# Kernel optimization log

Hardware: AMD Instinct MI355X
Metric: run time of the kernel (lower is better)

The kernel has to match this reference:

```python
import jax, jax.numpy as jnp
import numpy as np
from jax import lax

B, H = 4, 256          # batch, imsize
M1, M2 = 4096, 512     # total clusters at pooling level 1 / 2
E1, E2 = 65536, 8192   # coarsened edge counts
F = 64                 # node_feat_size (hard-coded in source)
HID = 100              # FCBlock hidden_ch


def _segment_mean(x, seg, n):
    s = jax.ops.segment_sum(x, seg, num_segments=n)
    c = jax.ops.segment_sum(jnp.ones((x.shape[0], 1), x.dtype), seg, num_segments=n)
    return s / jnp.maximum(c, 1.0)


def _fcblock(x, wi, bi, wh, bh, wo, bo):
    # FCBlock(hidden_ch=100, num_hidden_layers=3, outermost_linear=True)
    x = jax.nn.relu(x @ wi + bi)
    for k in range(wh.shape[0]):
        x = jax.nn.relu(x @ wh[k] + bh[k])
    return x @ wo + bo


def _graph_conv(x, ei, w_nei, w_self, b):
    # PyG GraphConv with aggr='mean': W_nei * mean_j x_j + W_self * x + b
    m = _segment_mean(x[ei[0]], ei[1], x.shape[0])
    return m @ w_nei + x @ w_self + b


def _render_qtr(G, feats):
    # feats: [N,20] = [centers(2), 3 channels x 6 quadratic params]
    centers = feats[:, :2]
    paras = feats[:, 2:].reshape(-1, 3, 6)
    dx = (G[:, 0] - centers[:, 0])[:, None]  # [N,1]
    dy = (G[:, 1] - centers[:, 1])[:, None]
    a, ah, aw, ahh, aww, ahw = (paras[:, :, k] for k in range(6))  # each [N,3]
    return a + ah * dx + aw * dy + ahh * dx ** 2 + aww * dy ** 2 + ahw * dx * dy


def setup_inputs() -> dict:
    key = jax.random.key(0)
    ks = iter(jax.random.split(key, 40))
    s = jnp.float32(0.05)
    d = {}
    d['img'] = jax.random.normal(next(ks), (B, H, H, 3), jnp.float32)
    d['conv_w'] = jax.random.normal(next(ks), (3, 3, 3, F), jnp.float32) * s
    d['conv_b'] = jax.random.normal(next(ks), (F,), jnp.float32) * s
    for p, din, dout in (('t1', F + 4, F), ('t2', F + 4, F), ('q', F, 18)):
        d[p + '_wi'] = jax.random.normal(next(ks), (din, HID), jnp.float32) * s
        d[p + '_bi'] = jax.random.normal(next(ks), (HID,), jnp.float32) * s
        d[p + '_wh'] = jax.random.normal(next(ks), (2, HID, HID), jnp.float32) * s
        d[p + '_bh'] = jax.random.normal(next(ks), (2, HID), jnp.float32) * s
        d[p + '_wo'] = jax.random.normal(next(ks), (HID, dout), jnp.float32) * s
        d[p + '_bo'] = jax.random.normal(next(ks), (dout,), jnp.float32) * s
    for p in ('gc1', 'gc2'):
        d[p + '_wn'] = jax.random.normal(next(ks), (F, F), jnp.float32) * s
        d[p + '_ws'] = jax.random.normal(next(ks), (F, F), jnp.float32) * s
        d[p + '_b'] = jax.random.normal(next(ks), (F,), jnp.float32) * s
    N = B * H * H
    d['cluster1'] = jax.random.randint(next(ks), (N,), 0, M1, jnp.int32)
    d['cluster2'] = jax.random.randint(next(ks), (M1,), 0, M2, jnp.int32)
    d['edges1'] = jax.random.randint(next(ks), (2, E1), 0, M1, jnp.int32)
    d['edges2'] = jax.random.randint(next(ks), (2, E2), 0, M2, jnp.int32)
    return d


def reference(img, conv_w, conv_b,
              t1_wi, t1_bi, t1_wh, t1_bh, t1_wo, t1_bo,
              t2_wi, t2_bi, t2_wh, t2_bh, t2_wo, t2_bo,
              q_wi, q_bi, q_wh, q_bh, q_wo, q_bo,
              gc1_wn, gc1_ws, gc1_b, gc2_wn, gc2_ws, gc2_b,
              cluster1, cluster2, edges1, edges2):
    b, h, w, _ = img.shape
    # RDN feature extractor stand-in: conv -> [B,H,W,F] -> flatten to pixel-nodes
    feats = lax.conv_general_dilated(img, conv_w, (1, 1), 'SAME',
                                     dimension_numbers=('NHWC', 'HWIO', 'NHWC')) + conv_b
    x = feats.reshape(-1, F)  # [N,F]
    ii, jj = jnp.meshgrid(jnp.arange(h), jnp.arange(w), indexing='ij')
    coords = jnp.stack([ii, jj], -1).reshape(-1, 2).astype(jnp.float32) / h
    coords = jnp.tile(coords, (b, 1))  # spatial_coords.repeat(batch,1)

    # ---- pooling level 1 ----
    x1 = _segment_mean(x, cluster1, M1)
    cen1 = _segment_mean(coords, cluster1, M1)
    mom1 = _segment_mean(coords ** 2, cluster1, M1)
    x1 = _fcblock(jnp.concatenate([x1, cen1, mom1], -1), t1_wi, t1_bi, t1_wh, t1_bh, t1_wo, t1_bo)
    x1 = _graph_conv(x1, edges1, gc1_wn, gc1_ws, gc1_b)

    # ---- pooling level 2 (composed cluster remap) ----
    cluster_r2 = cluster2[cluster1]  # pixel -> level-2 cluster
    x2 = _segment_mean(x1, cluster2, M2)
    cen2 = _segment_mean(coords, cluster_r2, M2)
    mom2 = _segment_mean(coords ** 2, cluster_r2, M2)
    x2 = _fcblock(jnp.concatenate([x2, cen2, mom2], -1), t2_wi, t2_bi, t2_wh, t2_bh, t2_wo, t2_bo)
    x2 = _graph_conv(x2, edges2, gc2_wn, gc2_ws, gc2_b)

    # ---- quadratic texture render per level ----
    jsf1 = jnp.concatenate([_fcblock(x1, q_wi, q_bi, q_wh, q_bh, q_wo, q_bo), cen1], -1)  # [M1,20]
    r1 = _render_qtr(coords, jsf1[cluster1]).reshape(b, h * w, 3)
    jsf2 = jnp.concatenate([_fcblock(x2, q_wi, q_bi, q_wh, q_bh, q_wo, q_bo), cen2], -1)  # [M2,20]
    r2 = _render_qtr(coords, jsf2[cluster_r2]).reshape(b, h * w, 3)
    return r1, r2, x1, x2
```

## Files before the change

### kernel.cpp

```cpp
#include <hip/hip_runtime.h>

#define NPIX 262144
#define M1C 4096
#define M2C 512
#define E1C 65536
#define E2C 8192
#define MROWS 8

constexpr int IOFF_H1   = 0;
constexpr int IOFF_HC2  = IOFF_H1  + M1C;
constexpr int IOFF_HE1  = IOFF_HC2 + M2C;
constexpr int IOFF_HE2  = IOFF_HE1 + M1C;
constexpr int ZEROI_END = IOFF_HE2 + M2C;

constexpr int IOFF_ST1   = ZEROI_END;
constexpr int IOFF_CU1   = IOFF_ST1  + M1C + 1;
constexpr int IOFF_STC2  = IOFF_CU1  + M1C;
constexpr int IOFF_CUC2  = IOFF_STC2 + M2C + 1;
constexpr int IOFF_STE1  = IOFF_CUC2 + M2C;
constexpr int IOFF_CUE1  = IOFF_STE1 + M1C + 1;
constexpr int IOFF_STE2  = IOFF_CUE1 + M1C;
constexpr int IOFF_CUE2  = IOFF_STE2 + M2C + 1;
constexpr int IOFF_PLIST = IOFF_CUE2 + M2C;
constexpr int IOFF_R2L   = IOFF_PLIST + NPIX;
constexpr int IOFF_E1L   = IOFF_R2L + M1C;
constexpr int IOFF_E2L   = IOFF_E1L + E1C;
constexpr int IEND       = IOFF_E2L + E2C;

constexpr int OFF_S1CR  = IEND;
constexpr int OFF_C1    = OFF_S1CR + M1C*4;
constexpr int OFF_X1CAT = OFF_C1 + M1C;
constexpr int OFF_X1FC  = OFF_X1CAT + M1C*68;
constexpr int OFF_X1    = OFF_X1FC + M1C*64;
constexpr int OFF_X2CAT = OFF_X1 + M1C*64;
constexpr int OFF_X2FC  = OFF_X2CAT + M2C*68;
constexpr int OFF_X2    = OFF_X2FC + M2C*64;
constexpr int OFF_JSF1  = OFF_X2 + M2C*64;
constexpr int OFF_JSF2  = OFF_JSF1 + M1C*20;

__global__ __launch_bounds__(256) void build_hist(
    const int* __restrict__ c1, const int* __restrict__ c2,
    const int* __restrict__ e1, const int* __restrict__ e2, int* __restrict__ wsI) {
  int i = blockIdx.x*256 + threadIdx.x;
  if (i < NPIX) {
    atomicAdd(&wsI[IOFF_H1 + c1[i]], 1);
  } else if (i < NPIX + M1C) {
    atomicAdd(&wsI[IOFF_HC2 + c2[i - NPIX]], 1);
  } else if (i < NPIX + M1C + E1C) {
    int e = i - NPIX - M1C;
    atomicAdd(&wsI[IOFF_HE1 + e1[E1C + e]], 1);
  } else {
    int e = i - NPIX - M1C - E1C;
    atomicAdd(&wsI[IOFF_HE2 + e2[E2C + e]], 1);
  }
}

__global__ __launch_bounds__(1024) void scan_kernel(int* __restrict__ wsI) {
  const int* hist; int* start; int* curs; int n;
  if (blockIdx.x == 0)      { hist = wsI+IOFF_H1;  start = wsI+IOFF_ST1;  curs = wsI+IOFF_CU1;  n = M1C; }
  else if (blockIdx.x == 1) { hist = wsI+IOFF_HC2; start = wsI+IOFF_STC2; curs = wsI+IOFF_CUC2; n = M2C; }
  else if (blockIdx.x == 2) { hist = wsI+IOFF_HE1; start = wsI+IOFF_STE1; curs = wsI+IOFF_CUE1; n = M1C; }
  else                      { hist = wsI+IOFF_HE2; start = wsI+IOFF_STE2; curs = wsI+IOFF_CUE2; n = M2C; }
  __shared__ int part[1024];
  int t = threadIdx.x, base = t*4, sum = 0;
  int loc0, loc1, loc2, loc3;
  loc0 = sum; sum += (base+0 < n) ? hist[base+0] : 0;
  loc1 = sum; sum += (base+1 < n) ? hist[base+1] : 0;
  loc2 = sum; sum += (base+2 < n) ? hist[base+2] : 0;
  loc3 = sum; sum += (base+3 < n) ? hist[base+3] : 0;
  part[t] = sum;
  __syncthreads();
  for (int off = 1; off < 1024; off <<= 1) {
    int v = (t >= off) ? part[t-off] : 0;
    __syncthreads();
    part[t] += v;
    __syncthreads();
  }
  int excl = (t == 0) ? 0 : part[t-1];
  if (base+0 < n) { start[base+0] = excl+loc0; curs[base+0] = excl+loc0; }
  if (base+1 < n) { start[base+1] = excl+loc1; curs[base+1] = excl+loc1; }
  if (base+2 < n) { start[base+2] = excl+loc2; curs[base+2] = excl+loc2; }
  if (base+3 < n) { start[base+3] = excl+loc3; curs[base+3] = excl+loc3; }
  if (t == 0) start[n] = part[1023];
}

__global__ __launch_bounds__(256) void scatter_all(
    const int* __restrict__ c1, const int* __restrict__ c2,
    const int* __restrict__ e1, const int* __restrict__ e2, int* __restrict__ wsI) {
  int i = blockIdx.x*256 + threadIdx.x;
  if (i < NPIX) {
    int s = c1[i];
    int pos = atomicAdd(&wsI[IOFF_CU1 + s], 1);
    wsI[IOFF_PLIST + pos] = i;
  } else if (i < NPIX + M1C) {
    int r = i - NPIX;
    int s = c2[r];
    int pos = atomicAdd(&wsI[IOFF_CUC2 + s], 1);
    wsI[IOFF_R2L + pos] = r;
  } else if (i < NPIX + M1C + E1C) {
    int e = i - NPIX - M1C;
    int d = e1[E1C + e];
    int pos = atomicAdd(&wsI[IOFF_CUE1 + d], 1);
    wsI[IOFF_E1L + pos] = e1[e];
  } else {
    int e = i - NPIX - M1C - E1C;
    int d = e2[E2C + e];
    int pos = atomicAdd(&wsI[IOFF_CUE2 + d], 1);
    wsI[IOFF_E2L + pos] = e2[e];
  }
}

__global__ __launch_bounds__(256) void gather_patch(
    const float* __restrict__ img, const float* __restrict__ cw, const float* __restrict__ cb,
    const int* __restrict__ start, const int* __restrict__ plist,
    float* __restrict__ x1cat, float* __restrict__ s1c_raw, float* __restrict__ c1f,
    float* __restrict__ jsf1) {
  int s = (blockIdx.x << 2) + (threadIdx.x >> 6);
  int l = threadIdx.x & 63;
  int p0 = start[s], p1 = start[s+1];
  int count = p1 - p0;
  float ps[27];
  #pragma unroll
  for (int k = 0; k < 27; ++k) ps[k] = 0.f;
  float sy = 0.f, sx = 0.f, syy = 0.f, sxx = 0.f;
  for (int p = p0 + l; p < p1; p += 64) {
    int n = plist[p];
    int b = n >> 16, pp = n & 65535, i = pp >> 8, j = pp & 255;
    #pragma unroll
    for (int di = 0; di < 3; ++di) {
      int y = i + di - 1;
      #pragma unroll
      for (int dj = 0; dj < 3; ++dj) {
        int x = j + dj - 1;
        int k = (di*3 + dj)*3;
        if ((unsigned)y < 256u && (unsigned)x < 256u) {
          int base = ((b << 16) + (y << 8) + x) * 3;
          ps[k+0] += img[base];
          ps[k+1] += img[base+1];
          ps[k+2] += img[base+2];
        }
      }
    }
    float yi = i * (1.0f/256.0f), xj = j * (1.0f/256.0f);
    sy += yi; sx += xj; syy += yi*yi; sxx += xj*xj;
  }
  #pragma unroll
  for (int m = 1; m < 64; m <<= 1) {
    #pragma unroll
    for (int k = 0; k < 27; ++k) ps[k] += __shfl_xor(ps[k], m);
    sy  += __shfl_xor(sy,  m);
    sx  += __shfl_xor(sx,  m);
    syy += __shfl_xor(syy, m);
    sxx += __shfl_xor(sxx, m);
  }
  float inv = 1.0f / fmaxf((float)count, 1.0f);
  float o = cb[l];
  #pragma unroll
  for (int k = 0; k < 27; ++k) o = fmaf(ps[k]*inv, cw[k*64 + l], o);
  x1cat[s*68 + l] = count ? o : 0.f;
  if (l == 0) {
    x1cat[s*68 + 64] = sy*inv;
    x1cat[s*68 + 65] = sx*inv;
    x1cat[s*68 + 66] = syy*inv;
    x1cat[s*68 + 67] = sxx*inv;
    s1c_raw[s*4+0] = sy; s1c_raw[s*4+1] = sx; s1c_raw[s*4+2] = syy; s1c_raw[s*4+3] = sxx;
    jsf1[s*20 + 18] = sy*inv;
    jsf1[s*20 + 19] = sx*inv;
    c1f[s] = (float)count;
  }
}

template<int NIN, int NOUT, int R, bool RELU>
__device__ __forceinline__ void block_layer(
    const float* __restrict__ W, const float* __restrict__ B,
    const float* __restrict__ actIn, float* __restrict__ actOut, int tid) {
  constexpr int NG  = 256 / NOUT;
  constexpr int RPT = (R + NG - 1) / NG;
  static_assert(NIN % 4 == 0, "NIN must be multiple of 4");
  int c  = tid % NOUT;
  int rg = tid / NOUT;
  if (rg < NG) {
    float acc[RPT];
    #pragma unroll
    for (int i = 0; i < RPT; ++i) acc[i] = 0.f;
    #pragma unroll 4
    for (int kc = 0; kc < NIN/4; ++kc) {
      float w0 = W[(kc*4+0)*NOUT + c];
      float w1 = W[(kc*4+1)*NOUT + c];
      float w2 = W[(kc*4+2)*NOUT + c];
      float w3 = W[(kc*4+3)*NOUT + c];
      #pragma unroll
      for (int i = 0; i < RPT; ++i) {
        int r = rg + i*NG;
        if (r < R) {
          float4 a = *reinterpret_cast<const float4*>(actIn + r*NIN + kc*4);
          acc[i] = fmaf(a.x, w0, fmaf(a.y, w1, fmaf(a.z, w2, fmaf(a.w, w3, acc[i]))));
        }
      }
    }
    float b = B[c];
    #pragma unroll
    for (int i = 0; i < RPT; ++i) {
      int r = rg + i*NG;
      if (r < R) {
        float v = acc[i] + b;
        actOut[r*NOUT + c] = RELU ? fmaxf(v, 0.f) : v;
      }
    }
  }
  __syncthreads();
}

__global__ __launch_bounds__(256) void mlp_t(
    const float* __restrict__ X, const float* __restrict__ wi, const float* __restrict__ bi,
    const float* __restrict__ wh, const float* __restrict__ bh,
    const float* __restrict__ wo, const float* __restrict__ bo,
    float* __restrict__ Y) {
  __shared__ float bufA[MROWS*100];
  __shared__ float bufB[MROWS*100];
  int tid = threadIdx.x;
  int r0 = blockIdx.x * MROWS;
  for (int o = tid; o < MROWS*68; o += 256) bufA[o] = X[r0*68 + o];
  __syncthreads();
  block_layer<68,100,MROWS,true>(wi, bi, bufA, bufB, tid);
  block_layer<100,100,MROWS,true>(wh, bh, bufB, bufA, tid);
  block_layer<100,100,MROWS,true>(wh+10000, bh+100, bufA, bufB, tid);
  block_layer<100,64,MROWS,false>(wo, bo, bufB, bufA, tid);
  for (int o = tid; o < MROWS*64; o += 256) Y[r0*64 + o] = bufA[o];
}

__global__ __launch_bounds__(256) void mlp_q(
    const float* __restrict__ X1, const float* __restrict__ X2,
    const float* __restrict__ wi, const float* __restrict__ bi,
    const float* __restrict__ wh, const float* __restrict__ bh,
    const float* __restrict__ wo, const float* __restrict__ bo,
    float* __restrict__ J1, float* __restrict__ J2) {
  __shared__ float bufA[MROWS*100];
  __shared__ float bufB[MROWS*100];
  int tid = threadIdx.x;
  const float* X; float* J; int r0;
  if (blockIdx.x < M1C/MROWS) { X = X1; J = J1; r0 = blockIdx.x * MROWS; }
  else                        { X = X2; J = J2; r0 = (blockIdx.x - M1C/MROWS) * MROWS; }
  for (int o = tid; o < MROWS*64; o += 256) bufA[o] = X[r0*64 + o];
  __syncthreads();
  block_layer<64,100,MROWS,true>(wi, bi, bufA, bufB, tid);
  block_layer<100,100,MROWS,true>(wh, bh, bufB, bufA, tid);
  block_layer<100,100,MROWS,true>(wh+10000, bh+100, bufA, bufB, tid);
  block_layer<100,18,MROWS,false>(wo, bo, bufB, bufA, tid);
  for (int o = tid; o < MROWS*18; o += 256) {
    int r = o / 18, c = o - r*18;
    J[(r0+r)*20 + c] = bufA[o];
  }
}

__global__ __launch_bounds__(64) void gc_fused(
    const int* __restrict__ start, const int* __restrict__ elist,
    const float* __restrict__ xin,
    const float* __restrict__ wn, const float* __restrict__ wsf, const float* __restrict__ bias,
    float* __restrict__ xout, float* __restrict__ out_f) {
  int d = blockIdx.x, c = threadIdx.x;
  int p0 = start[d], p1 = start[d+1];
  float acc = 0.f;
  for (int p = p0; p < p1; ++p) acc += xin[elist[p]*64 + c];
  float gm = acc / fmaxf((float)(p1 - p0), 1.0f);
  __shared__ float sm[128];
  sm[c] = gm;
  sm[64 + c] = xin[d*64 + c];
  __syncthreads();
  float o = bias[c];
  #pragma unroll
  for (int k = 0; k < 64; ++k)
    o += sm[k]*wn[k*64 + c] + sm[64 + k]*wsf[k*64 + c];
  xout[d*64 + c] = o;
  out_f[d*64 + c] = o;
}

__global__ __launch_bounds__(64) void pool_l2(
    const int* __restrict__ startc2, const int* __restrict__ r2list,
    const float* __restrict__ x1, const float* __restrict__ s1c_raw, const float* __restrict__ c1f,
    float* __restrict__ x2cat, float* __restrict__ jsf2) {
  int s2 = blockIdx.x, c = threadIdx.x;
  int p0 = startc2[s2], p1 = startc2[s2+1];
  int k = c & 3;
  float acc = 0.f, sc = 0.f, cnt = 0.f;
  for (int p = p0; p < p1; ++p) {
    int r = r2list[p];
    acc += x1[r*64 + c];
    sc  += s1c_raw[r*4 + k];
    cnt += c1f[r];
  }
  float invr = 1.0f / fmaxf((float)(p1 - p0), 1.0f);
  x2cat[s2*68 + c] = acc * invr;
  if (c < 4) {
    float mean = sc / fmaxf(cnt, 1.0f);
    x2cat[s2*68 + 64 + c] = mean;
    if (c == 0) jsf2[s2*20 + 18] = mean;
    if (c == 1) jsf2[s2*20 + 19] = mean;
  }
}

__global__ __launch_bounds__(256) void render_kernel(
    const int* __restrict__ cluster1, const int* __restrict__ cluster2,
    const float* __restrict__ jsf1, const float* __restrict__ jsf2,
    float* __restrict__ r1, float* __restrict__ r2) {
  int n = blockIdx.x*256 + threadIdx.x;
  int p = n & 65535, i = p >> 8, j = p & 255;
  float gy = i * (1.0f/256.0f), gx = j * (1.0f/256.0f);
  int s = cluster1[n];
  {
    const float4* f4 = reinterpret_cast<const float4*>(jsf1 + s*20);
    float4 v0 = f4[0], v1 = f4[1], v2 = f4[2], v3 = f4[3], v4 = f4[4];
    float dx = gy - v0.x, dy = gx - v0.y;
    float dxx = dx*dx, dyy = dy*dy, dxy = dx*dy;
    r1[n*3 + 0] = v0.z + v0.w*dx + v1.x*dy + v1.y*dxx + v1.z*dyy + v1.w*dxy;
    r1[n*3 + 1] = v2.x + v2.y*dx + v2.z*dy + v2.w*dxx + v3.x*dyy + v3.y*dxy;
    r1[n*3 + 2] = v3.z + v3.w*dx + v4.x*dy + v4.y*dxx + v4.z*dyy + v4.w*dxy;
  }
  int s2 = cluster2[s];
  {
    const float4* f4 = reinterpret_cast<const float4*>(jsf2 + s2*20);
    float4 v0 = f4[0], v1 = f4[1], v2 = f4[2], v3 = f4[3], v4 = f4[4];
    float dx = gy - v0.x, dy = gx - v0.y;
    float dxx = dx*dx, dyy = dy*dy, dxy = dx*dy;
    r2[n*3 + 0] = v0.z + v0.w*dx + v1.x*dy + v1.y*dxx + v1.z*dyy + v1.w*dxy;
    r2[n*3 + 1] = v2.x + v2.y*dx + v2.z*dy + v2.w*dxx + v3.x*dyy + v3.y*dxy;
    r2[n*3 + 2] = v3.z + v3.w*dx + v4.x*dy + v4.y*dxx + v4.z*dyy + v4.w*dxy;
  }
}

extern "C" void kernel_launch(void* const* d_in, const int* in_sizes, int n_in,
                              void* d_out, int out_size, void* d_ws, size_t ws_size,
                              hipStream_t stream) {
  const float* img    = (const float*)d_in[0];
  const float* conv_w = (const float*)d_in[1];
  const float* conv_b = (const float*)d_in[2];
  const float* t1_wi = (const float*)d_in[3];  const float* t1_bi = (const float*)d_in[4];
  const float* t1_wh = (const float*)d_in[5];  const float* t1_bh = (const float*)d_in[6];
  const float* t1_wo = (const float*)d_in[7];  const float* t1_bo = (const float*)d_in[8];
  const float* t2_wi = (const float*)d_in[9];  const float* t2_bi = (const float*)d_in[10];
  const float* t2_wh = (const float*)d_in[11]; const float* t2_bh = (const float*)d_in[12];
  const float* t2_wo = (const float*)d_in[13]; const float* t2_bo = (const float*)d_in[14];
  const float* q_wi  = (const float*)d_in[15]; const float* q_bi  = (const float*)d_in[16];
  const float* q_wh  = (const float*)d_in[17]; const float* q_bh  = (const float*)d_in[18];
  const float* q_wo  = (const float*)d_in[19]; const float* q_bo  = (const float*)d_in[20];
  const float* gc1_wn = (const float*)d_in[21]; const float* gc1_ws = (const float*)d_in[22];
  const float* gc1_b  = (const float*)d_in[23];
  const float* gc2_wn = (const float*)d_in[24]; const float* gc2_ws = (const float*)d_in[25];
  const float* gc2_b  = (const float*)d_in[26];
  const int* cluster1 = (const int*)d_in[27];
  const int* cluster2 = (const int*)d_in[28];
  const int* edges1   = (const int*)d_in[29];
  const int* edges2   = (const int*)d_in[30];

  float* ws = (float*)d_ws;
  int*   wsI = (int*)d_ws;
  float* out  = (float*)d_out;
  float* o_r1 = out;
  float* o_r2 = out + 786432;
  float* o_x1 = out + 1572864;
  float* o_x2 = out + 1835008;

  hipMemsetAsync(d_ws, 0, (size_t)ZEROI_END * sizeof(int), stream);

  constexpr int TOTW = NPIX + M1C + E1C + E2C;
  build_hist<<<TOTW/256, 256, 0, stream>>>(cluster1, cluster2, edges1, edges2, wsI);
  scan_kernel<<<4, 1024, 0, stream>>>(wsI);
  scatter_all<<<TOTW/256, 256, 0, stream>>>(cluster1, cluster2, edges1, edges2, wsI);

  gather_patch<<<M1C/4, 256, 0, stream>>>(img, conv_w, conv_b,
      wsI+IOFF_ST1, wsI+IOFF_PLIST,
      ws+OFF_X1CAT, ws+OFF_S1CR, ws+OFF_C1, ws+OFF_JSF1);

  mlp_t<<<M1C/MROWS, 256, 0, stream>>>(ws+OFF_X1CAT, t1_wi, t1_bi, t1_wh, t1_bh, t1_wo, t1_bo,
      ws+OFF_X1FC);

  gc_fused<<<M1C, 64, 0, stream>>>(wsI+IOFF_STE1, wsI+IOFF_E1L, ws+OFF_X1FC,
      gc1_wn, gc1_ws, gc1_b, ws+OFF_X1, o_x1);

  pool_l2<<<M2C, 64, 0, stream>>>(wsI+IOFF_STC2, wsI+IOFF_R2L,
      ws+OFF_X1, ws+OFF_S1CR, ws+OFF_C1, ws+OFF_X2CAT, ws+OFF_JSF2);

  mlp_t<<<M2C/MROWS, 256, 0, stream>>>(ws+OFF_X2CAT, t2_wi, t2_bi, t2_wh, t2_bh, t2_wo, t2_bo,
      ws+OFF_X2FC);

  gc_fused<<<M2C, 64, 0, stream>>>(wsI+IOFF_STE2, wsI+IOFF_E2L, ws+OFF_X2FC,
      gc2_wn, gc2_ws, gc2_b, ws+OFF_X2, o_x2);

  mlp_q<<<(M1C+M2C)/MROWS, 256, 0, stream>>>(ws+OFF_X1, ws+OFF_X2,
      q_wi, q_bi, q_wh, q_bh, q_wo, q_bo, ws+OFF_JSF1, ws+OFF_JSF2);

  render_kernel<<<NPIX/256, 256, 0, stream>>>(cluster1, cluster2, ws+OFF_JSF1, ws+OFF_JSF2, o_r1, o_r2);
}
```

Baseline: 177.7 us.

## Fuse gather/pool and graph-conv stages with their MLPs into four kernels

Merges each pooling or gather step with the following FCBlock MLP, and each graph-conv with the per-level texture MLP, so activations stay in shared memory. The launch sequence shrinks from seven mid-pipeline kernels to four, and intermediate concat buffers in workspace are removed. Each block now handles 4 rows instead of 8 in the MLP layers, which halves weight reuse per block but doubles block count. Level-2 kernels launch only 128 blocks.

```diff
diff --git a/kernel.cpp b/kernel.cpp
--- a/kernel.cpp
+++ b/kernel.cpp
@@ -5,7 +5,6 @@
 #define M2C 512
 #define E1C 65536
 #define E2C 8192
-#define MROWS 8
 
 constexpr int IOFF_H1   = 0;
 constexpr int IOFF_HC2  = IOFF_H1  + M1C;
@@ -25,17 +24,15 @@
 constexpr int IOFF_R2L   = IOFF_PLIST + NPIX;
 constexpr int IOFF_E1L   = IOFF_R2L + M1C;
 constexpr int IOFF_E2L   = IOFF_E1L + E1C;
-constexpr int IEND       = IOFF_E2L + E2C;
+constexpr int IEND0      = IOFF_E2L + E2C;
+constexpr int IEND       = (IEND0 + 3) & ~3;
 
 constexpr int OFF_S1CR  = IEND;
 constexpr int OFF_C1    = OFF_S1CR + M1C*4;
-constexpr int OFF_X1CAT = OFF_C1 + M1C;
-constexpr int OFF_X1FC  = OFF_X1CAT + M1C*68;
+constexpr int OFF_X1FC  = OFF_C1 + M1C;
 constexpr int OFF_X1    = OFF_X1FC + M1C*64;
-constexpr int OFF_X2CAT = OFF_X1 + M1C*64;
-constexpr int OFF_X2FC  = OFF_X2CAT + M2C*68;
-constexpr int OFF_X2    = OFF_X2FC + M2C*64;
-constexpr int OFF_JSF1  = OFF_X2 + M2C*64;
+constexpr int OFF_X2FC  = OFF_X1 + M1C*64;
+constexpr int OFF_JSF1  = OFF_X2FC + M2C*64;
 constexpr int OFF_JSF2  = OFF_JSF1 + M1C*20;
 
 __global__ __launch_bounds__(256) void build_hist(
@@ -94,79 +91,16 @@
     wsI[IOFF_PLIST + pos] = i;
   } else if (i < NPIX + M1C) {
     int r = i - NPIX;
-    int s = c2[r];
-    int pos = atomicAdd(&wsI[IOFF_CUC2 + s], 1);
+    int pos = atomicAdd(&wsI[IOFF_CUC2 + c2[r]], 1);
     wsI[IOFF_R2L + pos] = r;
   } else if (i < NPIX + M1C + E1C) {
     int e = i - NPIX - M1C;
-    int d = e1[E1C + e];
-    int pos = atomicAdd(&wsI[IOFF_CUE1 + d], 1);
+    int pos = atomicAdd(&wsI[IOFF_CUE1 + e1[E1C + e]], 1);
     wsI[IOFF_E1L + pos] = e1[e];
   } else {
     int e = i - NPIX - M1C - E1C;
-    int d = e2[E2C + e];
-    int pos = atomicAdd(&wsI[IOFF_CUE2 + d], 1);
+    int pos = atomicAdd(&wsI[IOFF_CUE2 + e2[E2C + e]], 1);
     wsI[IOFF_E2L + pos] = e2[e];
-  }
-}
-
-__global__ __launch_bounds__(256) void gather_patch(
-    const float* __restrict__ img, const float* __restrict__ cw, const float* __restrict__ cb,
-    const int* __restrict__ start, const int* __restrict__ plist,
-    float* __restrict__ x1cat, float* __restrict__ s1c_raw, float* __restrict__ c1f,
-    float* __restrict__ jsf1) {
-  int s = (blockIdx.x << 2) + (threadIdx.x >> 6);
-  int l = threadIdx.x & 63;
-  int p0 = start[s], p1 = start[s+1];
-  int count = p1 - p0;
-  float ps[27];
-  #pragma unroll
-  for (int k = 0; k < 27; ++k) ps[k] = 0.f;
-  float sy = 0.f, sx = 0.f, syy = 0.f, sxx = 0.f;
-  for (int p = p0 + l; p < p1; p += 64) {
-    int n = plist[p];
-    int b = n >> 16, pp = n & 65535, i = pp >> 8, j = pp & 255;
-    #pragma unroll
-    for (int di = 0; di < 3; ++di) {
-      int y = i + di - 1;
-      #pragma unroll
-      for (int dj = 0; dj < 3; ++dj) {
-        int x = j + dj - 1;
-        int k = (di*3 + dj)*3;
-        if ((unsigned)y < 256u && (unsigned)x < 256u) {
-          int base = ((b << 16) + (y << 8) + x) * 3;
-          ps[k+0] += img[base];
-          ps[k+1] += img[base+1];
-          ps[k+2] += img[base+2];
-        }
-      }
-    }
-    float yi = i * (1.0f/256.0f), xj = j * (1.0f/256.0f);
-    sy += yi; sx += xj; syy += yi*yi; sxx += xj*xj;
-  }
-  #pragma unroll
-  for (int m = 1; m < 64; m <<= 1) {
-    #pragma unroll
-    for (int k = 0; k < 27; ++k) ps[k] += __shfl_xor(ps[k], m);
-    sy  += __shfl_xor(sy,  m);
-    sx  += __shfl_xor(sx,  m);
-    syy += __shfl_xor(syy, m);
-    sxx += __shfl_xor(sxx, m);
-  }
-  float inv = 1.0f / fmaxf((float)count, 1.0f);
-  float o = cb[l];
-  #pragma unroll
-  for (int k = 0; k < 27; ++k) o = fmaf(ps[k]*inv, cw[k*64 + l], o);
-  x1cat[s*68 + l] = count ? o : 0.f;
-  if (l == 0) {
-    x1cat[s*68 + 64] = sy*inv;
-    x1cat[s*68 + 65] = sx*inv;
-    x1cat[s*68 + 66] = syy*inv;
-    x1cat[s*68 + 67] = sxx*inv;
-    s1c_raw[s*4+0] = sy; s1c_raw[s*4+1] = sx; s1c_raw[s*4+2] = syy; s1c_raw[s*4+3] = sxx;
-    jsf1[s*20 + 18] = sy*inv;
-    jsf1[s*20 + 19] = sx*inv;
-    c1f[s] = (float)count;
   }
 }
 
@@ -211,91 +145,186 @@
   __syncthreads();
 }
 
-__global__ __launch_bounds__(256) void mlp_t(
-    const float* __restrict__ X, const float* __restrict__ wi, const float* __restrict__ bi,
-    const float* __restrict__ wh, const float* __restrict__ bh,
-    const float* __restrict__ wo, const float* __restrict__ bo,
-    float* __restrict__ Y) {
-  __shared__ float bufA[MROWS*100];
-  __shared__ float bufB[MROWS*100];
-  int tid = threadIdx.x;
-  int r0 = blockIdx.x * MROWS;
-  for (int o = tid; o < MROWS*68; o += 256) bufA[o] = X[r0*68 + o];
-  __syncthreads();
-  block_layer<68,100,MROWS,true>(wi, bi, bufA, bufB, tid);
-  block_layer<100,100,MROWS,true>(wh, bh, bufB, bufA, tid);
-  block_layer<100,100,MROWS,true>(wh+10000, bh+100, bufA, bufB, tid);
-  block_layer<100,64,MROWS,false>(wo, bo, bufB, bufA, tid);
-  for (int o = tid; o < MROWS*64; o += 256) Y[r0*64 + o] = bufA[o];
-}
-
-__global__ __launch_bounds__(256) void mlp_q(
-    const float* __restrict__ X1, const float* __restrict__ X2,
-    const float* __restrict__ wi, const float* __restrict__ bi,
-    const float* __restrict__ wh, const float* __restrict__ bh,
-    const float* __restrict__ wo, const float* __restrict__ bo,
-    float* __restrict__ J1, float* __restrict__ J2) {
-  __shared__ float bufA[MROWS*100];
-  __shared__ float bufB[MROWS*100];
-  int tid = threadIdx.x;
-  const float* X; float* J; int r0;
-  if (blockIdx.x < M1C/MROWS) { X = X1; J = J1; r0 = blockIdx.x * MROWS; }
-  else                        { X = X2; J = J2; r0 = (blockIdx.x - M1C/MROWS) * MROWS; }
-  for (int o = tid; o < MROWS*64; o += 256) bufA[o] = X[r0*64 + o];
-  __syncthreads();
-  block_layer<64,100,MROWS,true>(wi, bi, bufA, bufB, tid);
-  block_layer<100,100,MROWS,true>(wh, bh, bufB, bufA, tid);
-  block_layer<100,100,MROWS,true>(wh+10000, bh+100, bufA, bufB, tid);
-  block_layer<100,18,MROWS,false>(wo, bo, bufB, bufA, tid);
-  for (int o = tid; o < MROWS*18; o += 256) {
-    int r = o / 18, c = o - r*18;
-    J[(r0+r)*20 + c] = bufA[o];
-  }
-}
-
-__global__ __launch_bounds__(64) void gc_fused(
-    const int* __restrict__ start, const int* __restrict__ elist,
+__global__ __launch_bounds__(256) void k1_gather_t1(
+    const float* __restrict__ img, const float* __restrict__ cw, const float* __restrict__ cb,
+    const int* __restrict__ start, const int* __restrict__ plist,
+    const float* t1_wi, const float* t1_bi, const float* t1_wh, const float* t1_bh,
+    const float* t1_wo, const float* t1_bo,
+    float* __restrict__ x1fc, float* __restrict__ s1c_raw, float* __restrict__ c1f,
+    float* __restrict__ jsf1) {
+  int tid = threadIdx.x, wv = tid >> 6, l = tid & 63;
+  int s = blockIdx.x*4 + wv;
+  __shared__ __align__(16) float bufA[4*100];
+  __shared__ __align__(16) float bufB[4*100];
+  int p0 = start[s], p1 = start[s+1];
+  int count = p1 - p0;
+  float ps[27];
+  #pragma unroll
+  for (int k = 0; k < 27; ++k) ps[k] = 0.f;
+  float sy = 0.f, sx = 0.f, syy = 0.f, sxx = 0.f;
+  for (int p = p0 + l; p < p1; p += 64) {
+    int n = plist[p];
+    int b = n >> 16, pp = n & 65535, i = pp >> 8, j = pp & 255;
+    #pragma unroll
+    for (int di = 0; di < 3; ++di) {
+      int y = i + di - 1;
+      #pragma unroll
+      for (int dj = 0; dj < 3; ++dj) {
+        int x = j + dj - 1;
+        int k = (di*3 + dj)*3;
+        if ((unsigned)y < 256u && (unsigned)x < 256u) {
+          int base = ((b << 16) + (y << 8) + x) * 3;
+          ps[k+0] += img[base];
+          ps[k+1] += img[base+1];
+          ps[k+2] += img[base+2];
+        }
+      }
+    }
+    float yi = i * (1.0f/256.0f), xj = j * (1.0f/256.0f);
+    sy += yi; sx += xj; syy += yi*yi; sxx += xj*xj;
+  }
+  #pragma unroll
+  for (int m = 1; m < 64; m <<= 1) {
+    #pragma unroll
+    for (int k = 0; k < 27; ++k) ps[k] += __shfl_xor(ps[k], m);
+    sy  += __shfl_xor(sy,  m);
+    sx  += __shfl_xor(sx,  m);
+    syy += __shfl_xor(syy, m);
+    sxx += __shfl_xor(sxx, m);
+  }
+  float inv = 1.0f / fmaxf((float)count, 1.0f);
+  float o = cb[l];
+  #pragma unroll
+  for (int k = 0; k < 27; ++k) o = fmaf(ps[k]*inv, cw[k*64 + l], o);
+  bufA[wv*68 + l] = count ? o : 0.f;
+  if (l == 0) {
+    bufA[wv*68 + 64] = sy*inv;
+    bufA[wv*68 + 65] = sx*inv;
+    bufA[wv*68 + 66] = syy*inv;
+    bufA[wv*68 + 67] = sxx*inv;
+    s1c_raw[s*4+0] = sy; s1c_raw[s*4+1] = sx;
+    s1c_raw[s*4+2] = syy; s1c_raw[s*4+3] = sxx;
+    jsf1[s*20 + 18] = sy*inv;
+    jsf1[s*20 + 19] = sx*inv;
+    c1f[s] = (float)count;
+  }
+  __syncthreads();
+  block_layer<68,100,4,true>(t1_wi, t1_bi, bufA, bufB, tid);
+  block_layer<100,100,4,true>(t1_wh, t1_bh, bufB, bufA, tid);
+  block_layer<100,100,4,true>(t1_wh+10000, t1_bh+100, bufA, bufB, tid);
+  block_layer<100,64,4,false>(t1_wo, t1_bo, bufB, bufA, tid);
+  int r0 = blockIdx.x*4;
+  for (int o2 = tid; o2 < 4*64; o2 += 256) x1fc[r0*64 + o2] = bufA[o2];
+}
+
+__global__ __launch_bounds__(256) void k2_gc1_q(
+    const int* __restrict__ startE, const int* __restrict__ elist,
     const float* __restrict__ xin,
-    const float* __restrict__ wn, const float* __restrict__ wsf, const float* __restrict__ bias,
-    float* __restrict__ xout, float* __restrict__ out_f) {
-  int d = blockIdx.x, c = threadIdx.x;
-  int p0 = start[d], p1 = start[d+1];
+    const float* wn, const float* wsf, const float* bias,
+    const float* q_wi, const float* q_bi, const float* q_wh, const float* q_bh,
+    const float* q_wo, const float* q_bo,
+    float* __restrict__ x1_ws, float* __restrict__ out_f, float* __restrict__ jsf) {
+  int tid = threadIdx.x, wv = tid >> 6, l = tid & 63;
+  int d = blockIdx.x*4 + wv;
+  __shared__ __align__(16) float bufA[4*100];
+  __shared__ __align__(16) float bufB[4*100];
+  __shared__ float smW[4*128];
+  float* sm = smW + wv*128;
+  int p0 = startE[d], p1 = startE[d+1];
   float acc = 0.f;
-  for (int p = p0; p < p1; ++p) acc += xin[elist[p]*64 + c];
-  float gm = acc / fmaxf((float)(p1 - p0), 1.0f);
-  __shared__ float sm[128];
-  sm[c] = gm;
-  sm[64 + c] = xin[d*64 + c];
-  __syncthreads();
-  float o = bias[c];
-  #pragma unroll
+  for (int p = p0; p < p1; ++p) acc += xin[elist[p]*64 + l];
+  sm[l]      = acc / fmaxf((float)(p1 - p0), 1.0f);
+  sm[64 + l] = xin[d*64 + l];
+  __syncthreads();
+  float o = bias[l];
+  #pragma unroll 8
   for (int k = 0; k < 64; ++k)
-    o += sm[k]*wn[k*64 + c] + sm[64 + k]*wsf[k*64 + c];
-  xout[d*64 + c] = o;
-  out_f[d*64 + c] = o;
-}
-
-__global__ __launch_bounds__(64) void pool_l2(
+    o += sm[k]*wn[k*64 + l] + sm[64 + k]*wsf[k*64 + l];
+  x1_ws[d*64 + l] = o;
+  out_f[d*64 + l] = o;
+  bufA[wv*64 + l] = o;
+  __syncthreads();
+  block_layer<64,100,4,true>(q_wi, q_bi, bufA, bufB, tid);
+  block_layer<100,100,4,true>(q_wh, q_bh, bufB, bufA, tid);
+  block_layer<100,100,4,true>(q_wh+10000, q_bh+100, bufA, bufB, tid);
+  block_layer<100,18,4,false>(q_wo, q_bo, bufB, bufA, tid);
+  int r0 = blockIdx.x*4;
+  for (int o2 = tid; o2 < 4*18; o2 += 256) {
+    int r = o2 / 18, c = o2 - r*18;
+    jsf[(r0+r)*20 + c] = bufA[o2];
+  }
+}
+
+__global__ __launch_bounds__(256) void k3_pool_t2(
     const int* __restrict__ startc2, const int* __restrict__ r2list,
     const float* __restrict__ x1, const float* __restrict__ s1c_raw, const float* __restrict__ c1f,
-    float* __restrict__ x2cat, float* __restrict__ jsf2) {
-  int s2 = blockIdx.x, c = threadIdx.x;
+    const float* t2_wi, const float* t2_bi, const float* t2_wh, const float* t2_bh,
+    const float* t2_wo, const float* t2_bo,
+    float* __restrict__ x2fc, float* __restrict__ jsf2) {
+  int tid = threadIdx.x, wv = tid >> 6, l = tid & 63;
+  int s2 = blockIdx.x*4 + wv;
+  __shared__ __align__(16) float bufA[4*100];
+  __shared__ __align__(16) float bufB[4*100];
   int p0 = startc2[s2], p1 = startc2[s2+1];
-  int k = c & 3;
+  int k = l & 3;
   float acc = 0.f, sc = 0.f, cnt = 0.f;
   for (int p = p0; p < p1; ++p) {
     int r = r2list[p];
-    acc += x1[r*64 + c];
+    acc += x1[r*64 + l];
     sc  += s1c_raw[r*4 + k];
     cnt += c1f[r];
   }
   float invr = 1.0f / fmaxf((float)(p1 - p0), 1.0f);
-  x2cat[s2*68 + c] = acc * invr;
-  if (c < 4) {
+  bufA[wv*68 + l] = acc * invr;
+  if (l < 4) {
     float mean = sc / fmaxf(cnt, 1.0f);
-    x2cat[s2*68 + 64 + c] = mean;
-    if (c == 0) jsf2[s2*20 + 18] = mean;
-    if (c == 1) jsf2[s2*20 + 19] = mean;
+    bufA[wv*68 + 64 + l] = mean;
+    if (l == 0) jsf2[s2*20 + 18] = mean;
+    if (l == 1) jsf2[s2*20 + 19] = mean;
+  }
+  __syncthreads();
+  block_layer<68,100,4,true>(t2_wi, t2_bi, bufA, bufB, tid);
+  block_layer<100,100,4,true>(t2_wh, t2_bh, bufB, bufA, tid);
+  block_layer<100,100,4,true>(t2_wh+10000, t2_bh+100, bufA, bufB, tid);
+  block_layer<100,64,4,false>(t2_wo, t2_bo, bufB, bufA, tid);
+  int r0 = blockIdx.x*4;
+  for (int o2 = tid; o2 < 4*64; o2 += 256) x2fc[r0*64 + o2] = bufA[o2];
+}
+
+__global__ __launch_bounds__(256) void k4_gc2_q(
+    const int* __restrict__ startE, const int* __restrict__ elist,
+    const float* __restrict__ xin,
+    const float* wn, const float* wsf, const float* bias,
+    const float* q_wi, const float* q_bi, const float* q_wh, const float* q_bh,
+    const float* q_wo, const float* q_bo,
+    float* __restrict__ out_f, float* __restrict__ jsf2) {
+  int tid = threadIdx.x, wv = tid >> 6, l = tid & 63;
+  int d = blockIdx.x*4 + wv;
+  __shared__ __align__(16) float bufA[4*100];
+  __shared__ __align__(16) float bufB[4*100];
+  __shared__ float smW[4*128];
+  float* sm = smW + wv*128;
+  int p0 = startE[d], p1 = startE[d+1];
+  float acc = 0.f;
+  for (int p = p0; p < p1; ++p) acc += xin[elist[p]*64 + l];
+  sm[l]      = acc / fmaxf((float)(p1 - p0), 1.0f);
+  sm[64 + l] = xin[d*64 + l];
+  __syncthreads();
+  float o = bias[l];
+  #pragma unroll 8
+  for (int k = 0; k < 64; ++k)
+    o += sm[k]*wn[k*64 + l] + sm[64 + k]*wsf[k*64 + l];
+  out_f[d*64 + l] = o;
+  bufA[wv*64 + l] = o;
+  __syncthreads();
+  block_layer<64,100,4,true>(q_wi, q_bi, bufA, bufB, tid);
+  block_layer<100,100,4,true>(q_wh, q_bh, bufB, bufA, tid);
+  block_layer<100,100,4,true>(q_wh+10000, q_bh+100, bufA, bufB, tid);
+  block_layer<100,18,4,false>(q_wo, q_bo, bufB, bufA, tid);
+  int r0 = blockIdx.x*4;
+  for (int o2 = tid; o2 < 4*18; o2 += 256) {
+    int r = o2 / 18, c = o2 - r*18;
+    jsf2[(r0+r)*20 + c] = bufA[o2];
   }
 }
 
@@ -367,27 +396,25 @@
   scan_kernel<<<4, 1024, 0, stream>>>(wsI);
   scatter_all<<<TOTW/256, 256, 0, stream>>>(cluster1, cluster2, edges1, edges2, wsI);
 
-  gather_patch<<<M1C/4, 256, 0, stream>>>(img, conv_w, conv_b,
+  k1_gather_t1<<<M1C/4, 256, 0, stream>>>(img, conv_w, conv_b,
       wsI+IOFF_ST1, wsI+IOFF_PLIST,
-      ws+OFF_X1CAT, ws+OFF_S1CR, ws+OFF_C1, ws+OFF_JSF1);
-
-  mlp_t<<<M1C/MROWS, 256, 0, stream>>>(ws+OFF_X1CAT, t1_wi, t1_bi, t1_wh, t1_bh, t1_wo, t1_bo,
-      ws+OFF_X1FC);
-
-  gc_fused<<<M1C, 64, 0, stream>>>(wsI+IOFF_STE1, wsI+IOFF_E1L, ws+OFF_X1FC,
-      gc1_wn, gc1_ws, gc1_b, ws+OFF_X1, o_x1);
-
-  pool_l2<<<M2C, 64, 0, stream>>>(wsI+IOFF_STC2, wsI+IOFF_R2L,
-      ws+OFF_X1, ws+OFF_S1CR, ws+OFF_C1, ws+OFF_X2CAT, ws+OFF_JSF2);
-
-  mlp_t<<<M2C/MROWS, 256, 0, stream>>>(ws+OFF_X2CAT, t2_wi, t2_bi, t2_wh, t2_bh, t2_wo, t2_bo,
-      ws+OFF_X2FC);
-
-  gc_fused<<<M2C, 64, 0, stream>>>(wsI+IOFF_STE2, wsI+IOFF_E2L, ws+OFF_X2FC,
-      gc2_wn, gc2_ws, gc2_b, ws+OFF_X2, o_x2);
-
-  mlp_q<<<(M1C+M2C)/MROWS, 256, 0, stream>>>(ws+OFF_X1, ws+OFF_X2,
-      q_wi, q_bi, q_wh, q_bh, q_wo, q_bo, ws+OFF_JSF1, ws+OFF_JSF2);
+      t1_wi, t1_bi, t1_wh, t1_bh, t1_wo, t1_bo,
+      ws+OFF_X1FC, ws+OFF_S1CR, ws+OFF_C1, ws+OFF_JSF1);
+
+  k2_gc1_q<<<M1C/4, 256, 0, stream>>>(wsI+IOFF_STE1, wsI+IOFF_E1L, ws+OFF_X1FC,
+      gc1_wn, gc1_ws, gc1_b,
+      q_wi, q_bi, q_wh, q_bh, q_wo, q_bo,
+      ws+OFF_X1, o_x1, ws+OFF_JSF1);
+
+  k3_pool_t2<<<M2C/4, 256, 0, stream>>>(wsI+IOFF_STC2, wsI+IOFF_R2L,
+      ws+OFF_X1, ws+OFF_S1CR, ws+OFF_C1,
+      t2_wi, t2_bi, t2_wh, t2_bh, t2_wo, t2_bo,
+      ws+OFF_X2FC, ws+OFF_JSF2);
+
+  k4_gc2_q<<<M2C/4, 256, 0, stream>>>(wsI+IOFF_STE2, wsI+IOFF_E2L, ws+OFF_X2FC,
+      gc2_wn, gc2_ws, gc2_b,
+      q_wi, q_bi, q_wh, q_bh, q_wo, q_bo,
+      o_x2, ws+OFF_JSF2);
 
   render_kernel<<<NPIX/256, 256, 0, stream>>>(cluster1, cluster2, ws+OFF_JSF1, ws+OFF_JSF2, o_r1, o_r2);
 }
```

New measurement: 180.3 us. About the same (+1.5%).
